# Optimization experiments

Measured on AMD Instinct MI355X. Metric: run time of the kernel, lower is better.

The kernel has to match this reference:

```python
import jax, jax.numpy as jnp
import numpy as np
import math

N_HEADS = 8
D_EMBED = 512
D_CROSS = 768
FF_DIM = 2048
D_HEAD = D_EMBED // N_HEADS


def _gelu_tanh(x):
    # matches the module's hand-written tanh GELU
    return 0.5 * x * (1.0 + jnp.tanh(jnp.sqrt(2.0 / jnp.pi) * (x + 0.044715 * x ** 3)))


def _layer_norm(x, g, b, eps=1e-5):
    mu = jnp.mean(x, axis=-1, keepdims=True)
    var = jnp.var(x, axis=-1, keepdims=True)
    return (x - mu) * jax.lax.rsqrt(var + eps) * g + b


def setup_inputs() -> dict:
    key = jax.random.key(0)
    ks = jax.random.split(key, 20)
    s = 0.02
    inp = {
        "x": jax.random.normal(ks[0], (2, 4096, D_EMBED), jnp.float32),
        "y": jax.random.normal(ks[1], (2, 77, D_CROSS), jnp.float32),
        # self-attention: fused in_proj [D, 3D]
        "sa_in_w": jax.random.normal(ks[2], (D_EMBED, 3 * D_EMBED), jnp.float32) * s,
        "sa_in_b": jnp.zeros((3 * D_EMBED,), jnp.float32),
        "sa_out_w": jax.random.normal(ks[3], (D_EMBED, D_EMBED), jnp.float32) * s,
        "sa_out_b": jnp.zeros((D_EMBED,), jnp.float32),
        # cross-attention
        "ca_q_w": jax.random.normal(ks[4], (D_EMBED, D_EMBED), jnp.float32) * s,
        "ca_q_b": jnp.zeros((D_EMBED,), jnp.float32),
        "ca_k_w": jax.random.normal(ks[5], (D_CROSS, D_EMBED), jnp.float32) * s,
        "ca_k_b": jnp.zeros((D_EMBED,), jnp.float32),
        "ca_v_w": jax.random.normal(ks[6], (D_CROSS, D_EMBED), jnp.float32) * s,
        "ca_v_b": jnp.zeros((D_EMBED,), jnp.float32),
        "ca_out_w": jax.random.normal(ks[7], (D_EMBED, D_EMBED), jnp.float32) * s,
        "ca_out_b": jnp.zeros((D_EMBED,), jnp.float32),
        # feed-forward
        "ff_w1": jax.random.normal(ks[8], (D_EMBED, FF_DIM), jnp.float32) * s,
        "ff_b1": jnp.zeros((FF_DIM,), jnp.float32),
        "ff_w2": jax.random.normal(ks[9], (FF_DIM, D_EMBED), jnp.float32) * s,
        "ff_b2": jnp.zeros((D_EMBED,), jnp.float32),
        # layer norms
        "ln1_g": jnp.ones((D_EMBED,), jnp.float32),
        "ln1_b": jnp.zeros((D_EMBED,), jnp.float32),
        "ln2_g": jnp.ones((D_EMBED,), jnp.float32),
        "ln2_b": jnp.zeros((D_EMBED,), jnp.float32),
        "ln3_g": jnp.ones((D_EMBED,), jnp.float32),
        "ln3_b": jnp.zeros((D_EMBED,), jnp.float32),
    }
    return inp


def _mha(q, k, v):
    # q,k,v: [B, S, D] -> split heads -> attention -> merge
    B, Sq, D = q.shape
    Skv = k.shape[1]
    qh = q.reshape(B, Sq, N_HEADS, D_HEAD).transpose(0, 2, 1, 3)
    kh = k.reshape(B, Skv, N_HEADS, D_HEAD).transpose(0, 2, 1, 3)
    vh = v.reshape(B, Skv, N_HEADS, D_HEAD).transpose(0, 2, 1, 3)
    scores = jnp.einsum("bhqd,bhkd->bhqk", qh, kh) / math.sqrt(D_HEAD)
    w = jax.nn.softmax(scores, axis=-1)
    out = jnp.einsum("bhqk,bhkd->bhqd", w, vh)
    return out.transpose(0, 2, 1, 3).reshape(B, Sq, D)


def reference(x, y, sa_in_w, sa_in_b, sa_out_w, sa_out_b,
              ca_q_w, ca_q_b, ca_k_w, ca_k_b, ca_v_w, ca_v_b, ca_out_w, ca_out_b,
              ff_w1, ff_b1, ff_w2, ff_b2,
              ln1_g, ln1_b, ln2_g, ln2_b, ln3_g, ln3_b):
    # self-attention (no causal mask; default causal_mask=False)
    qkv = x @ sa_in_w + sa_in_b
    q, k, v = jnp.split(qkv, 3, axis=-1)
    sa = _mha(q, k, v) @ sa_out_w + sa_out_b
    x = _layer_norm(x + sa, ln1_g, ln1_b)

    # cross-attention to y
    qc = x @ ca_q_w + ca_q_b
    kc = y @ ca_k_w + ca_k_b
    vc = y @ ca_v_w + ca_v_b
    ca = _mha(qc, kc, vc) @ ca_out_w + ca_out_b
    x = _layer_norm(x + ca, ln2_g, ln2_b)

    # feed-forward with tanh GELU
    ff = _gelu_tanh(x @ ff_w1 + ff_b1) @ ff_w2 + ff_b2
    x = _layer_norm(x + ff, ln3_g, ln3_b)
    return x
```

## Files before the change

### kernel.cpp

```cpp
#include <hip/hip_runtime.h>
#include <stdint.h>

typedef float floatx4 __attribute__((ext_vector_type(4)));
typedef __bf16 bf16x8 __attribute__((ext_vector_type(8)));
typedef unsigned int uintx4 __attribute__((ext_vector_type(4)));
typedef unsigned short ushort_t;

__device__ __forceinline__ float b2f(ushort_t u) {
  union { unsigned int i; float f; } x; x.i = ((unsigned int)u) << 16; return x.f;
}
__device__ __forceinline__ ushort_t f2b(float f) {
  union { float f; unsigned int i; } x; x.f = f;
  unsigned int i = x.i;
  return (ushort_t)((i + 0x7FFFu + ((i >> 16) & 1u)) >> 16);
}
__device__ __forceinline__ unsigned fbits(float f) {
  union { float f; unsigned u; } x; x.f = f; return x.u;
}
__device__ __forceinline__ uintx4 ld16(const void* p) {
  uintx4 v; __builtin_memcpy(&v, p, 16); return v;
}
__device__ __forceinline__ void st16(void* p, uintx4 v) { __builtin_memcpy(p, &v, 16); }
__device__ __forceinline__ floatx4 f4splat(float x) { floatx4 v = {x, x, x, x}; return v; }
__device__ __forceinline__ void sched_fence() { asm volatile("" ::: "memory"); }

__device__ __forceinline__ floatx4 mfma16(uintx4 a, uintx4 b, floatx4 c) {
  return __builtin_amdgcn_mfma_f32_16x16x32_bf16(
      __builtin_bit_cast(bf16x8, a), __builtin_bit_cast(bf16x8, b), c, 0, 0, 0);
}

__device__ __forceinline__ void gll16(const ushort_t* g, ushort_t* l) {
  __builtin_amdgcn_global_load_lds(
      (__attribute__((address_space(1))) void*)(g),
      (__attribute__((address_space(3))) void*)(l), 16, 0, 0);
}

template <int EPI>
__global__ __launch_bounds__(256, 2) void gemm_bt(
    const ushort_t* __restrict__ A, const ushort_t* __restrict__ Bt,
    const float* __restrict__ bias, void* __restrict__ Cout,
    int N, int K) {
  __shared__ alignas(16) ushort_t lA[128 * 32];
  __shared__ alignas(16) ushort_t lB[128 * 32];
  const int tid = threadIdx.x;
  const int wave = tid >> 6, lane = tid & 63;
  const int quad = lane >> 4, l16 = lane & 15;
  const int bm = blockIdx.y * 128, bn = blockIdx.x * 128;
  const int wm = (wave >> 1) * 64, wn = (wave & 1) * 64;

  const ushort_t* ag0 = A + (size_t)(bm + wave * 32 + (lane >> 2)) * K + (lane & 3) * 8;
  const ushort_t* ag1 = ag0 + (size_t)16 * K;
  const ushort_t* bg0 = Bt + (size_t)(bn + wave * 32 + (lane >> 2)) * K + (lane & 3) * 8;
  const ushort_t* bg1 = bg0 + (size_t)16 * K;
  ushort_t* la = lA + wave * 1024;
  ushort_t* lb = lB + wave * 1024;

  floatx4 acc[4][4];
#pragma unroll
  for (int i = 0; i < 4; i++)
#pragma unroll
    for (int j = 0; j < 4; j++) acc[i][j] = f4splat(0.f);

  for (int k0 = 0; k0 < K; k0 += 32) {
    __syncthreads();
    gll16(ag0 + k0, la);
    gll16(ag1 + k0, la + 512);
    gll16(bg0 + k0, lb);
    gll16(bg1 + k0, lb + 512);
    __syncthreads();
    uintx4 af[4], bf[4];
#pragma unroll
    for (int i = 0; i < 4; i++) af[i] = ld16(&lA[(wm + i * 16 + l16) * 32 + quad * 8]);
#pragma unroll
    for (int i = 0; i < 4; i++) bf[i] = ld16(&lB[(wn + i * 16 + l16) * 32 + quad * 8]);
#pragma unroll
    for (int mi = 0; mi < 4; mi++)
#pragma unroll
      for (int ni = 0; ni < 4; ni++) acc[mi][ni] = mfma16(af[mi], bf[ni], acc[mi][ni]);
  }

  float bv[4];
#pragma unroll
  for (int ni = 0; ni < 4; ni++) bv[ni] = bias[bn + wn + ni * 16 + l16];

#pragma unroll
  for (int mi = 0; mi < 4; mi++)
#pragma unroll
    for (int ni = 0; ni < 4; ni++)
#pragma unroll
      for (int r = 0; r < 4; r++) {
        int row = bm + wm + mi * 16 + quad * 4 + r;
        int col = bn + wn + ni * 16 + l16;
        float v = acc[mi][ni][r] + bv[ni];
        if (EPI == 2) {
          float w = v + 0.044715f * v * v * v;
          float e = __builtin_amdgcn_exp2f(-2.3022084f * w);
          v = v * __builtin_amdgcn_rcpf(1.f + e);
        }
        if (EPI == 1)
          ((float*)Cout)[(size_t)row * N + col] = v;
        else
          ((ushort_t*)Cout)[(size_t)row * N + col] = f2b(v);
      }
}

__global__ __launch_bounds__(256, 2) void flash_self(
    const ushort_t* __restrict__ qkv, const ushort_t* __restrict__ vt,
    ushort_t* __restrict__ outp) {
  __shared__ alignas(16) ushort_t lK[64 * 72];
  __shared__ alignas(16) ushort_t lV[64 * 72];
  __shared__ alignas(16) ushort_t lPT[4 * 32 * 72];
  const int tid = threadIdx.x, wave = tid >> 6, lane = tid & 63;
  const int quad = lane >> 4, l16 = lane & 15;
  const int bh = blockIdx.x, b = bh >> 3, h = bh & 7;
  const int qt = blockIdx.y;

  const ushort_t* Qb = qkv + (size_t)b * 4096 * 1536 + h * 64;
  const ushort_t* Kb = Qb + 512;
  const ushort_t* Vtb = vt + (size_t)bh * 64 * 4096;

  uintx4 qf[2][2];
#pragma unroll
  for (int mi = 0; mi < 2; mi++)
#pragma unroll
    for (int kf = 0; kf < 2; kf++)
      qf[mi][kf] = ld16(Qb + (size_t)(qt * 128 + wave * 32 + mi * 16 + l16) * 1536 +
                        kf * 32 + quad * 8);

  floatx4 O[2][4];
#pragma unroll
  for (int mi = 0; mi < 2; mi++)
#pragma unroll
    for (int dn = 0; dn < 4; dn++) O[mi][dn] = f4splat(0.f);
  float lsum[2] = {0.f, 0.f};
  const float c = 0.18033688f;

  const int sr0 = tid >> 3, sr1 = 32 + (tid >> 3), sc0 = (tid & 7) * 8;
  uintx4 kr0 = ld16(Kb + (size_t)sr0 * 1536 + sc0);
  uintx4 kr1 = ld16(Kb + (size_t)sr1 * 1536 + sc0);
  uintx4 vr0 = ld16(Vtb + (size_t)sr0 * 4096 + sc0);
  uintx4 vr1 = ld16(Vtb + (size_t)sr1 * 4096 + sc0);

  ushort_t* PTw = lPT + wave * 32 * 72;

  for (int kt = 0; kt < 64; kt++) {
    __syncthreads();
    st16(&lK[sr0 * 72 + sc0], kr0);
    st16(&lK[sr1 * 72 + sc0], kr1);
    st16(&lV[sr0 * 72 + sc0], vr0);
    st16(&lV[sr1 * 72 + sc0], vr1);
    __syncthreads();

    int ktn = (kt + 1) & 63;
    kr0 = ld16(Kb + (size_t)(ktn * 64 + sr0) * 1536 + sc0);
    kr1 = ld16(Kb + (size_t)(ktn * 64 + sr1) * 1536 + sc0);
    vr0 = ld16(Vtb + (size_t)sr0 * 4096 + ktn * 64 + sc0);
    vr1 = ld16(Vtb + (size_t)sr1 * 4096 + ktn * 64 + sc0);

    floatx4 S[2][4];
#pragma unroll
    for (int ni = 0; ni < 4; ni++) {
      uintx4 k0 = ld16(&lK[(ni * 16 + l16) * 72 + quad * 8]);
      uintx4 k1 = ld16(&lK[(ni * 16 + l16) * 72 + 32 + quad * 8]);
#pragma unroll
      for (int mi = 0; mi < 2; mi++) {
        floatx4 z = f4splat(0.f);
        z = mfma16(k0, qf[mi][0], z);
        z = mfma16(k1, qf[mi][1], z);
        S[mi][ni] = z;
      }
    }

#pragma unroll
    for (int mi = 0; mi < 2; mi++) {
      float rs = 0.f;
#pragma unroll
      for (int ni = 0; ni < 4; ni++) {
        float p0 = __builtin_amdgcn_exp2f(S[mi][ni][0] * c);
        float p1 = __builtin_amdgcn_exp2f(S[mi][ni][1] * c);
        float p2 = __builtin_amdgcn_exp2f(S[mi][ni][2] * c);
        float p3 = __builtin_amdgcn_exp2f(S[mi][ni][3] * c);
        rs += (p0 + p1) + (p2 + p3);
        unsigned dd[2];
        dd[0] = (fbits(p1) & 0xFFFF0000u) | (fbits(p0) >> 16);
        dd[1] = (fbits(p3) & 0xFFFF0000u) | (fbits(p2) >> 16);
        __builtin_memcpy(&PTw[(mi * 16 + l16) * 72 + ni * 16 + quad * 4], dd, 8);
      }
      lsum[mi] += rs;
    }
    sched_fence();

#pragma unroll
    for (int f = 0; f < 2; f++) {
      uintx4 pf0 = ld16(&PTw[(0 + l16) * 72 + f * 32 + quad * 8]);
      uintx4 pf1 = ld16(&PTw[(16 + l16) * 72 + f * 32 + quad * 8]);
#pragma unroll
      for (int dn = 0; dn < 4; dn++) {
        uintx4 vb = ld16(&lV[(dn * 16 + l16) * 72 + f * 32 + quad * 8]);
        O[0][dn] = mfma16(vb, pf0, O[0][dn]);
        O[1][dn] = mfma16(vb, pf1, O[1][dn]);
      }
    }
  }

#pragma unroll
  for (int mi = 0; mi < 2; mi++) {
    lsum[mi] += __shfl_xor(lsum[mi], 16);
    lsum[mi] += __shfl_xor(lsum[mi], 32);
  }

#pragma unroll
  for (int mi = 0; mi < 2; mi++) {
    float inv = 1.0f / lsum[mi];
    const size_t rowg = (size_t)b * 4096 + qt * 128 + wave * 32 + mi * 16 + l16;
#pragma unroll
    for (int dn = 0; dn < 4; dn++) {
      unsigned u0 = (unsigned)f2b(O[mi][dn][0] * inv) | ((unsigned)f2b(O[mi][dn][1] * inv) << 16);
      unsigned u1 = (unsigned)f2b(O[mi][dn][2] * inv) | ((unsigned)f2b(O[mi][dn][3] * inv) << 16);
      unsigned uu[2] = {u0, u1};
      __builtin_memcpy(outp + rowg * 512 + h * 64 + dn * 16 + quad * 4, uu, 8);
    }
  }
}

__global__ __launch_bounds__(256, 2) void cross_attn(
    const ushort_t* __restrict__ qc, const ushort_t* __restrict__ kc,
    const ushort_t* __restrict__ vc, ushort_t* __restrict__ outp) {
  __shared__ alignas(16) ushort_t lK[96 * 72];
  __shared__ alignas(16) ushort_t lV[64 * 104];
  __shared__ alignas(16) ushort_t lP[128 * 104];
  const int tid = threadIdx.x, wave = tid >> 6, lane = tid & 63;
  const int quad = lane >> 4, l16 = lane & 15;
  const int bh = blockIdx.y, b = bh >> 3, h = bh & 7;
  const int qt = blockIdx.x;

#pragma unroll
  for (int i = 0; i < 3; i++) {
    int ch = i * 256 + tid;
    int r = ch >> 3, c8 = ch & 7;
    uintx4 d = {0u, 0u, 0u, 0u};
    if (r < 77) d = ld16(kc + (size_t)(b * 77 + r) * 512 + h * 64 + c8 * 8);
    st16(&lK[r * 72 + c8 * 8], d);
  }
  for (int i = 0; i < 24; i++) {
    int e = i * 256 + tid;
    int dd = e / 96, s = e - dd * 96;
    ushort_t v = 0;
    if (s < 77) v = vc[(size_t)(b * 77 + s) * 512 + h * 64 + dd];
    lV[dd * 104 + s] = v;
  }
  __syncthreads();

  const int qr0 = qt * 128 + wave * 32;
  uintx4 qf[2][2];
#pragma unroll
  for (int mi = 0; mi < 2; mi++)
#pragma unroll
    for (int kf = 0; kf < 2; kf++)
      qf[mi][kf] =
          ld16(qc + (size_t)(b * 4096 + qr0 + mi * 16 + l16) * 512 + h * 64 + kf * 32 + quad * 8);

  floatx4 S[2][6];
#pragma unroll
  for (int ni = 0; ni < 6; ni++) {
    uintx4 k0 = ld16(&lK[(ni * 16 + l16) * 72 + quad * 8]);
    uintx4 k1 = ld16(&lK[(ni * 16 + l16) * 72 + 32 + quad * 8]);
#pragma unroll
    for (int mi = 0; mi < 2; mi++) {
      floatx4 z = f4splat(0.f);
      z = mfma16(qf[mi][0], k0, z);
      z = mfma16(qf[mi][1], k1, z);
      S[mi][ni] = z;
    }
  }
  const float c = 0.18033688f;
#pragma unroll
  for (int ni = 4; ni < 6; ni++)
    if (ni * 16 + l16 >= 77) {
      S[0][ni] = f4splat(-1e30f);
      S[1][ni] = f4splat(-1e30f);
    }

  floatx4 linv[2];
#pragma unroll
  for (int mi = 0; mi < 2; mi++) {
    floatx4 cm = S[mi][0];
#pragma unroll
    for (int ni = 1; ni < 6; ni++)
#pragma unroll
      for (int r = 0; r < 4; r++) cm[r] = fmaxf(cm[r], S[mi][ni][r]);
#pragma unroll
    for (int off = 1; off < 16; off <<= 1)
#pragma unroll
      for (int r = 0; r < 4; r++) cm[r] = fmaxf(cm[r], __shfl_xor(cm[r], off));
    floatx4 rs = f4splat(0.f);
#pragma unroll
    for (int ni = 0; ni < 6; ni++)
#pragma unroll
      for (int r = 0; r < 4; r++) {
        float p = __builtin_amdgcn_exp2f(S[mi][ni][r] * c - cm[r] * c);
        S[mi][ni][r] = p;
        rs[r] += p;
      }
#pragma unroll
    for (int off = 1; off < 16; off <<= 1)
#pragma unroll
      for (int r = 0; r < 4; r++) rs[r] += __shfl_xor(rs[r], off);
#pragma unroll
    for (int r = 0; r < 4; r++) linv[mi][r] = 1.0f / rs[r];
#pragma unroll
    for (int ni = 0; ni < 6; ni++)
#pragma unroll
      for (int r = 0; r < 4; r++)
        lP[(wave * 32 + mi * 16 + quad * 4 + r) * 104 + ni * 16 + l16] = f2b(S[mi][ni][r]);
  }
  sched_fence();

  floatx4 O[2][4];
#pragma unroll
  for (int mi = 0; mi < 2; mi++)
#pragma unroll
    for (int dn = 0; dn < 4; dn++) O[mi][dn] = f4splat(0.f);
#pragma unroll
  for (int kf = 0; kf < 3; kf++) {
    uintx4 pa0 = ld16(&lP[(wave * 32 + 0 + l16) * 104 + kf * 32 + quad * 8]);
    uintx4 pa1 = ld16(&lP[(wave * 32 + 16 + l16) * 104 + kf * 32 + quad * 8]);
#pragma unroll
    for (int dn = 0; dn < 4; dn++) {
      uintx4 vb = ld16(&lV[(dn * 16 + l16) * 104 + kf * 32 + quad * 8]);
      O[0][dn] = mfma16(pa0, vb, O[0][dn]);
      O[1][dn] = mfma16(pa1, vb, O[1][dn]);
    }
  }
#pragma unroll
  for (int mi = 0; mi < 2; mi++)
#pragma unroll
    for (int dn = 0; dn < 4; dn++)
#pragma unroll
      for (int r = 0; r < 4; r++) {
        int row = b * 4096 + qt * 128 + wave * 32 + mi * 16 + quad * 4 + r;
        int col = h * 64 + dn * 16 + l16;
        outp[(size_t)row * 512 + col] = f2b(O[mi][dn][r] * linv[mi][r]);
      }
}

template <int RESF>
__global__ __launch_bounds__(256) void ln_kernel(
    const float* __restrict__ p, const void* __restrict__ resv,
    const float* __restrict__ g, const float* __restrict__ bb,
    float* __restrict__ out32, ushort_t* __restrict__ outbf) {
  const int row = blockIdx.x * 4 + (threadIdx.x >> 6);
  const int lane = threadIdx.x & 63;
  const size_t base = (size_t)row * 512;
  float v[8];
  float s = 0.f, ss = 0.f;
#pragma unroll
  for (int i = 0; i < 4; i++) {
    int cidx = i * 128 + lane * 2;
    float2 pv; __builtin_memcpy(&pv, p + base + cidx, 8);
    float rx, ry;
    if (RESF) {
      float2 rv; __builtin_memcpy(&rv, (const float*)resv + base + cidx, 8);
      rx = rv.x; ry = rv.y;
    } else {
      unsigned int rr; __builtin_memcpy(&rr, (const ushort_t*)resv + base + cidx, 4);
      rx = b2f((ushort_t)(rr & 0xFFFFu));
      ry = b2f((ushort_t)(rr >> 16));
    }
    float a = pv.x + rx, b2 = pv.y + ry;
    v[2 * i] = a; v[2 * i + 1] = b2;
    s += a + b2;
    ss += a * a + b2 * b2;
  }
#pragma unroll
  for (int off = 1; off < 64; off <<= 1) {
    s += __shfl_xor(s, off);
    ss += __shfl_xor(ss, off);
  }
  float mean = s * (1.f / 512.f);
  float var = ss * (1.f / 512.f) - mean * mean;
  float rstd = rsqrtf(var + 1e-5f);
#pragma unroll
  for (int i = 0; i < 4; i++) {
    int cidx = i * 128 + lane * 2;
    float2 gv; __builtin_memcpy(&gv, g + cidx, 8);
    float2 bv; __builtin_memcpy(&bv, bb + cidx, 8);
    float y0 = (v[2 * i] - mean) * rstd * gv.x + bv.x;
    float y1 = (v[2 * i + 1] - mean) * rstd * gv.y + bv.y;
    if (out32) {
      float2 o; o.x = y0; o.y = y1;
      __builtin_memcpy(out32 + base + cidx, &o, 8);
    }
    if (outbf) {
      unsigned int o16 = (unsigned int)f2b(y0) | ((unsigned int)f2b(y1) << 16);
      __builtin_memcpy(outbf + base + cidx, &o16, 4);
    }
  }
}

__global__ __launch_bounds__(256) void small_gemm2(
    const float* __restrict__ y, const float* __restrict__ wk,
    const float* __restrict__ bk, const float* __restrict__ wv,
    const float* __restrict__ bv, ushort_t* __restrict__ kout,
    ushort_t* __restrict__ vout) {
  int bid = blockIdx.x;
  const float* W; const float* B; ushort_t* O;
  if (bid >= 308) { W = wv; B = bv; O = vout; bid -= 308; }
  else            { W = wk; B = bk; O = kout; }
  int idx = bid * 256 + threadIdx.x;
  if (idx >= 154 * 512) return;
  int r = idx >> 9, col = idx & 511;
  const float* ya = y + (size_t)r * 768;
  float acc = B[col];
#pragma unroll 4
  for (int k = 0; k < 768; k++) acc += ya[k] * W[(size_t)k * 512 + col];
  O[idx] = f2b(acc);
}

struct TransJob { const float* in; ushort_t* out; int ldi, ldo, nbx, start; };
struct TransJobs6 { TransJob j[6]; };

__global__ __launch_bounds__(256) void transpose6(TransJobs6 jobs) {
  __shared__ float t[32][33];
  int bid = blockIdx.x;
  int ji = 0;
#pragma unroll
  for (int i = 1; i < 6; i++)
    if (bid >= jobs.j[i].start) ji = i;
  TransJob J = jobs.j[ji];
  int local = bid - J.start;
  int by = local / J.nbx, bx = local - by * J.nbx;
  int r0 = by * 32, c0 = bx * 32;
  int tx = threadIdx.x & 31, ty = threadIdx.x >> 5;
#pragma unroll
  for (int i = 0; i < 4; i++)
    t[ty + 8 * i][tx] = J.in[(size_t)(r0 + ty + 8 * i) * J.ldi + c0 + tx];
  __syncthreads();
#pragma unroll
  for (int i = 0; i < 4; i++)
    J.out[(size_t)(c0 + ty + 8 * i) * J.ldo + r0 + tx] = f2b(t[tx][ty + 8 * i]);
}

__global__ __launch_bounds__(256) void xcvt(const float* __restrict__ in,
                                            ushort_t* __restrict__ out) {
  int i = (blockIdx.x * 256 + threadIdx.x) * 4;
  float4 v; __builtin_memcpy(&v, in + i, 16);
  ushort_t o[4] = {f2b(v.x), f2b(v.y), f2b(v.z), f2b(v.w)};
  __builtin_memcpy(out + i, o, 8);
}

__global__ __launch_bounds__(256) void transpose_v(const ushort_t* __restrict__ qkv,
                                                   ushort_t* __restrict__ vt) {
  __shared__ ushort_t t[32][33];
  int b = blockIdx.z;
  const ushort_t* in = qkv + (size_t)b * 4096 * 1536 + 1024;
  ushort_t* out = vt + (size_t)b * 512 * 4096;
  int r0 = blockIdx.y * 32, c0 = blockIdx.x * 32;
  int tx = threadIdx.x & 31, ty = threadIdx.x >> 5;
#pragma unroll
  for (int i = 0; i < 4; i++)
    t[ty + 8 * i][tx] = in[(size_t)(r0 + ty + 8 * i) * 1536 + c0 + tx];
  __syncthreads();
#pragma unroll
  for (int i = 0; i < 4; i++)
    out[(size_t)(c0 + ty + 8 * i) * 4096 + r0 + tx] = t[tx][ty + 8 * i];
}

extern "C" void kernel_launch(void* const* d_in, const int* in_sizes, int n_in,
                              void* d_out, int out_size, void* d_ws, size_t ws_size,
                              hipStream_t stream) {
  const size_t MiB = 1048576;
  if (ws_size < 64 * MiB) return;

  const float* x        = (const float*)d_in[0];
  const float* y        = (const float*)d_in[1];
  const float* sa_in_w  = (const float*)d_in[2];
  const float* sa_in_b  = (const float*)d_in[3];
  const float* sa_out_w = (const float*)d_in[4];
  const float* sa_out_b = (const float*)d_in[5];
  const float* ca_q_w   = (const float*)d_in[6];
  const float* ca_q_b   = (const float*)d_in[7];
  const float* ca_k_w   = (const float*)d_in[8];
  const float* ca_k_b   = (const float*)d_in[9];
  const float* ca_v_w   = (const float*)d_in[10];
  const float* ca_v_b   = (const float*)d_in[11];
  const float* ca_out_w = (const float*)d_in[12];
  const float* ca_out_b = (const float*)d_in[13];
  const float* ff_w1    = (const float*)d_in[14];
  const float* ff_b1    = (const float*)d_in[15];
  const float* ff_w2    = (const float*)d_in[16];
  const float* ff_b2    = (const float*)d_in[17];
  const float* ln1_g    = (const float*)d_in[18];
  const float* ln1_b    = (const float*)d_in[19];
  const float* ln2_g    = (const float*)d_in[20];
  const float* ln2_b    = (const float*)d_in[21];
  const float* ln3_g    = (const float*)d_in[22];
  const float* ln3_b    = (const float*)d_in[23];

  char* w = (char*)d_ws;
  ushort_t* QKV  = (ushort_t*)(w + 0);
  float*    P    = (float*)(w + 0);
  ushort_t* QC   = (ushort_t*)(w + 0);
  float*    P2   = (float*)(w + 0);
  ushort_t* FF   = (ushort_t*)(w + 0);
  ushort_t* ATT  = (ushort_t*)(w + 24 * MiB);
  ushort_t* VT   = (ushort_t*)(w + 32 * MiB);
  float*    XB0  = (float*)(w + 32 * MiB);
  float*    P3   = (float*)(w + 32 * MiB);
  ushort_t* XBF  = (ushort_t*)(w + 48 * MiB);
  ushort_t* XB0b = (ushort_t*)(w + 48 * MiB);
  ushort_t* XB1b = (ushort_t*)(w + 48 * MiB);
  ushort_t* WT   = (ushort_t*)(w + 56 * MiB);
  ushort_t* KC   = (ushort_t*)(w + 63 * MiB);
  ushort_t* VC   = KC + 154 * 512;

  ushort_t* WT_sain  = WT;
  ushort_t* WT_saout = WT_sain + 786432;
  ushort_t* WT_caq   = WT_saout + 262144;
  ushort_t* WT_caout = WT_caq + 262144;
  ushort_t* WT_ff1   = WT_caout + 262144;
  ushort_t* WT_ff2   = WT_ff1 + 1048576;

  TransJobs6 tj;
  tj.j[0] = TransJob{sa_in_w,  WT_sain,  1536, 512, 48, 0};
  tj.j[1] = TransJob{sa_out_w, WT_saout, 512,  512, 16, 768};
  tj.j[2] = TransJob{ca_q_w,   WT_caq,   512,  512, 16, 1024};
  tj.j[3] = TransJob{ca_out_w, WT_caout, 512,  512, 16, 1280};
  tj.j[4] = TransJob{ff_w1,    WT_ff1,   2048, 512, 64, 1536};
  tj.j[5] = TransJob{ff_w2,    WT_ff2,   512, 2048, 16, 2560};
  transpose6<<<3584, 256, 0, stream>>>(tj);
  xcvt<<<4096, 256, 0, stream>>>(x, XBF);

  gemm_bt<0><<<dim3(12, 64), 256, 0, stream>>>(XBF, WT_sain, sa_in_b, QKV, 1536, 512);
  transpose_v<<<dim3(16, 128, 2), 256, 0, stream>>>(QKV, VT);
  flash_self<<<dim3(16, 32), 256, 0, stream>>>(QKV, VT, ATT);
  gemm_bt<1><<<dim3(4, 64), 256, 0, stream>>>(ATT, WT_saout, sa_out_b, P, 512, 512);
  ln_kernel<1><<<2048, 256, 0, stream>>>(P, x, ln1_g, ln1_b, XB0, XB0b);

  gemm_bt<0><<<dim3(4, 64), 256, 0, stream>>>(XB0b, WT_caq, ca_q_b, QC, 512, 512);
  small_gemm2<<<616, 256, 0, stream>>>(y, ca_k_w, ca_k_b, ca_v_w, ca_v_b, KC, VC);
  cross_attn<<<dim3(32, 16), 256, 0, stream>>>(QC, KC, VC, ATT);
  gemm_bt<1><<<dim3(4, 64), 256, 0, stream>>>(ATT, WT_caout, ca_out_b, P2, 512, 512);
  ln_kernel<1><<<2048, 256, 0, stream>>>(P2, XB0, ln2_g, ln2_b, nullptr, XB1b);

  gemm_bt<2><<<dim3(16, 64), 256, 0, stream>>>(XB1b, WT_ff1, ff_b1, FF, 2048, 512);
  gemm_bt<1><<<dim3(4, 64), 256, 0, stream>>>(FF, WT_ff2, ff_b2, P3, 512, 2048);
  ln_kernel<0><<<2048, 256, 0, stream>>>(P3, XB1b, ln3_g, ln3_b, (float*)d_out, nullptr);
}
```

Baseline: 466.8 us.

## Pre-pack K/V into MFMA fragment layout, narrow GEMM tiles, vectorize layernorm

Self-attention K and V are repacked by two new kernels into per-lane MFMA fragment order, so flash_self loads fragments straight from global memory and drops its LDS staging and both per-tile barriers. The N=512 GEMMs switch to a 64-wide N tile, which doubles the grid to 512 blocks and fills the GPU better. Layernorm now uses 16-byte loads and stores. In exchange there are two extra packing launches and more global traffic in the attention inner loop, now served through cache instead of LDS.

```diff
diff --git a/kernel.cpp b/kernel.cpp
--- a/kernel.cpp
+++ b/kernel.cpp
@@ -35,58 +35,67 @@
       (__attribute__((address_space(3))) void*)(l), 16, 0, 0);
 }
 
-template <int EPI>
+template <int EPI, int NT>
 __global__ __launch_bounds__(256, 2) void gemm_bt(
     const ushort_t* __restrict__ A, const ushort_t* __restrict__ Bt,
     const float* __restrict__ bias, void* __restrict__ Cout,
     int N, int K) {
+  constexpr int NI = NT / 32;
   __shared__ alignas(16) ushort_t lA[128 * 32];
-  __shared__ alignas(16) ushort_t lB[128 * 32];
+  __shared__ alignas(16) ushort_t lB[NT * 32];
   const int tid = threadIdx.x;
   const int wave = tid >> 6, lane = tid & 63;
   const int quad = lane >> 4, l16 = lane & 15;
-  const int bm = blockIdx.y * 128, bn = blockIdx.x * 128;
-  const int wm = (wave >> 1) * 64, wn = (wave & 1) * 64;
+  const int bm = blockIdx.y * 128, bn = blockIdx.x * NT;
+  const int wm = (wave >> 1) * 64, wn = (wave & 1) * (NT / 2);
 
   const ushort_t* ag0 = A + (size_t)(bm + wave * 32 + (lane >> 2)) * K + (lane & 3) * 8;
   const ushort_t* ag1 = ag0 + (size_t)16 * K;
-  const ushort_t* bg0 = Bt + (size_t)(bn + wave * 32 + (lane >> 2)) * K + (lane & 3) * 8;
-  const ushort_t* bg1 = bg0 + (size_t)16 * K;
   ushort_t* la = lA + wave * 1024;
-  ushort_t* lb = lB + wave * 1024;
-
-  floatx4 acc[4][4];
+  const ushort_t* bg0;
+  const ushort_t* bg1 = nullptr;
+  ushort_t* lb;
+  if (NT == 128) {
+    bg0 = Bt + (size_t)(bn + wave * 32 + (lane >> 2)) * K + (lane & 3) * 8;
+    bg1 = bg0 + (size_t)16 * K;
+    lb = lB + wave * 1024;
+  } else {
+    bg0 = Bt + (size_t)(bn + wave * 16 + (lane >> 2)) * K + (lane & 3) * 8;
+    lb = lB + wave * 512;
+  }
+
+  floatx4 acc[4][NI];
 #pragma unroll
   for (int i = 0; i < 4; i++)
 #pragma unroll
-    for (int j = 0; j < 4; j++) acc[i][j] = f4splat(0.f);
+    for (int j = 0; j < NI; j++) acc[i][j] = f4splat(0.f);
 
   for (int k0 = 0; k0 < K; k0 += 32) {
     __syncthreads();
     gll16(ag0 + k0, la);
     gll16(ag1 + k0, la + 512);
     gll16(bg0 + k0, lb);
-    gll16(bg1 + k0, lb + 512);
+    if (NT == 128) gll16(bg1 + k0, lb + 512);
     __syncthreads();
-    uintx4 af[4], bf[4];
+    uintx4 af[4], bf[NI];
 #pragma unroll
     for (int i = 0; i < 4; i++) af[i] = ld16(&lA[(wm + i * 16 + l16) * 32 + quad * 8]);
 #pragma unroll
-    for (int i = 0; i < 4; i++) bf[i] = ld16(&lB[(wn + i * 16 + l16) * 32 + quad * 8]);
+    for (int i = 0; i < NI; i++) bf[i] = ld16(&lB[(wn + i * 16 + l16) * 32 + quad * 8]);
 #pragma unroll
     for (int mi = 0; mi < 4; mi++)
 #pragma unroll
-      for (int ni = 0; ni < 4; ni++) acc[mi][ni] = mfma16(af[mi], bf[ni], acc[mi][ni]);
-  }
-
-  float bv[4];
-#pragma unroll
-  for (int ni = 0; ni < 4; ni++) bv[ni] = bias[bn + wn + ni * 16 + l16];
+      for (int ni = 0; ni < NI; ni++) acc[mi][ni] = mfma16(af[mi], bf[ni], acc[mi][ni]);
+  }
+
+  float bv[NI];
+#pragma unroll
+  for (int ni = 0; ni < NI; ni++) bv[ni] = bias[bn + wn + ni * 16 + l16];
 
 #pragma unroll
   for (int mi = 0; mi < 4; mi++)
 #pragma unroll
-    for (int ni = 0; ni < 4; ni++)
+    for (int ni = 0; ni < NI; ni++)
 #pragma unroll
       for (int r = 0; r < 4; r++) {
         int row = bm + wm + mi * 16 + quad * 4 + r;
@@ -104,11 +113,52 @@
       }
 }
 
+__global__ __launch_bounds__(256) void pack_k(const ushort_t* __restrict__ qkv,
+                                              ushort_t* __restrict__ KP) {
+  int g = blockIdx.x * 256 + threadIdx.x;
+  int lane = g & 63;
+  int frag = (g >> 6) & 7;
+  int kt = (g >> 9) & 63;
+  int bh = g >> 15;
+  int b = bh >> 3, h = bh & 7;
+  int ni = frag >> 1, kf = frag & 1;
+  int l16 = lane & 15, quad = lane >> 4;
+  const ushort_t* src = qkv + (size_t)(b * 4096 + kt * 64 + ni * 16 + l16) * 1536 +
+                        512 + h * 64 + kf * 32 + quad * 8;
+  st16(KP + (size_t)g * 8, ld16(src));
+}
+
+__global__ __launch_bounds__(256) void pack_v(const ushort_t* __restrict__ qkv,
+                                              ushort_t* __restrict__ VP) {
+  __shared__ ushort_t t[64 * 72];
+  int bh = blockIdx.x, kt = blockIdx.y;
+  int b = bh >> 3, h = bh & 7;
+  int tid = threadIdx.x;
+#pragma unroll
+  for (int i = 0; i < 2; i++) {
+    int c = i * 256 + tid;
+    int row = c >> 3, c8 = (c & 7) * 8;
+    uintx4 d4 = ld16(qkv + (size_t)(b * 4096 + kt * 64 + row) * 1536 + 1024 + h * 64 + c8);
+    ushort_t tmp[8];
+    __builtin_memcpy(tmp, &d4, 16);
+#pragma unroll
+    for (int j = 0; j < 8; j++) t[(c8 + j) * 72 + row] = tmp[j];
+  }
+  __syncthreads();
+#pragma unroll
+  for (int i = 0; i < 2; i++) {
+    int c = i * 256 + tid;
+    int frag = c >> 6, lane = c & 63;
+    int f = frag >> 2, dn = frag & 3;
+    int l16 = lane & 15, quad = lane >> 4;
+    uintx4 d4 = ld16(&t[(dn * 16 + l16) * 72 + f * 32 + quad * 8]);
+    st16(VP + ((size_t)(bh * 64 + kt) * 8 + frag) * 512 + (size_t)lane * 8, d4);
+  }
+}
+
 __global__ __launch_bounds__(256, 2) void flash_self(
-    const ushort_t* __restrict__ qkv, const ushort_t* __restrict__ vt,
-    ushort_t* __restrict__ outp) {
-  __shared__ alignas(16) ushort_t lK[64 * 72];
-  __shared__ alignas(16) ushort_t lV[64 * 72];
+    const ushort_t* __restrict__ qkv, const ushort_t* __restrict__ KP,
+    const ushort_t* __restrict__ VP, ushort_t* __restrict__ outp) {
   __shared__ alignas(16) ushort_t lPT[4 * 32 * 72];
   const int tid = threadIdx.x, wave = tid >> 6, lane = tid & 63;
   const int quad = lane >> 4, l16 = lane & 15;
@@ -116,8 +166,8 @@
   const int qt = blockIdx.y;
 
   const ushort_t* Qb = qkv + (size_t)b * 4096 * 1536 + h * 64;
-  const ushort_t* Kb = Qb + 512;
-  const ushort_t* Vtb = vt + (size_t)bh * 64 * 4096;
+  const ushort_t* KPb = KP + (size_t)bh * 64 * 4096;
+  const ushort_t* VPb = VP + (size_t)bh * 64 * 4096;
 
   uintx4 qf[2][2];
 #pragma unroll
@@ -134,42 +184,36 @@
     for (int dn = 0; dn < 4; dn++) O[mi][dn] = f4splat(0.f);
   float lsum[2] = {0.f, 0.f};
   const float c = 0.18033688f;
-
-  const int sr0 = tid >> 3, sr1 = 32 + (tid >> 3), sc0 = (tid & 7) * 8;
-  uintx4 kr0 = ld16(Kb + (size_t)sr0 * 1536 + sc0);
-  uintx4 kr1 = ld16(Kb + (size_t)sr1 * 1536 + sc0);
-  uintx4 vr0 = ld16(Vtb + (size_t)sr0 * 4096 + sc0);
-  uintx4 vr1 = ld16(Vtb + (size_t)sr1 * 4096 + sc0);
-
   ushort_t* PTw = lPT + wave * 32 * 72;
 
+#pragma unroll 2
   for (int kt = 0; kt < 64; kt++) {
-    __syncthreads();
-    st16(&lK[sr0 * 72 + sc0], kr0);
-    st16(&lK[sr1 * 72 + sc0], kr1);
-    st16(&lV[sr0 * 72 + sc0], vr0);
-    st16(&lV[sr1 * 72 + sc0], vr1);
-    __syncthreads();
-
-    int ktn = (kt + 1) & 63;
-    kr0 = ld16(Kb + (size_t)(ktn * 64 + sr0) * 1536 + sc0);
-    kr1 = ld16(Kb + (size_t)(ktn * 64 + sr1) * 1536 + sc0);
-    vr0 = ld16(Vtb + (size_t)sr0 * 4096 + ktn * 64 + sc0);
-    vr1 = ld16(Vtb + (size_t)sr1 * 4096 + ktn * 64 + sc0);
+    const ushort_t* kb = KPb + kt * 4096;
+    uintx4 kfr[4][2];
+#pragma unroll
+    for (int ni = 0; ni < 4; ni++)
+#pragma unroll
+      for (int kf = 0; kf < 2; kf++)
+        kfr[ni][kf] = ld16(kb + ((ni * 2 + kf) * 64 + lane) * 8);
 
     floatx4 S[2][4];
 #pragma unroll
-    for (int ni = 0; ni < 4; ni++) {
-      uintx4 k0 = ld16(&lK[(ni * 16 + l16) * 72 + quad * 8]);
-      uintx4 k1 = ld16(&lK[(ni * 16 + l16) * 72 + 32 + quad * 8]);
+    for (int ni = 0; ni < 4; ni++)
 #pragma unroll
       for (int mi = 0; mi < 2; mi++) {
         floatx4 z = f4splat(0.f);
-        z = mfma16(k0, qf[mi][0], z);
-        z = mfma16(k1, qf[mi][1], z);
+        z = mfma16(kfr[ni][0], qf[mi][0], z);
+        z = mfma16(kfr[ni][1], qf[mi][1], z);
         S[mi][ni] = z;
       }
-    }
+
+    const ushort_t* vbp = VPb + kt * 4096;
+    uintx4 vf[2][4];
+#pragma unroll
+    for (int f = 0; f < 2; f++)
+#pragma unroll
+      for (int dn = 0; dn < 4; dn++)
+        vf[f][dn] = ld16(vbp + ((f * 4 + dn) * 64 + lane) * 8);
 
 #pragma unroll
     for (int mi = 0; mi < 2; mi++) {
@@ -196,9 +240,8 @@
       uintx4 pf1 = ld16(&PTw[(16 + l16) * 72 + f * 32 + quad * 8]);
 #pragma unroll
       for (int dn = 0; dn < 4; dn++) {
-        uintx4 vb = ld16(&lV[(dn * 16 + l16) * 72 + f * 32 + quad * 8]);
-        O[0][dn] = mfma16(vb, pf0, O[0][dn]);
-        O[1][dn] = mfma16(vb, pf1, O[1][dn]);
+        O[0][dn] = mfma16(vf[f][dn], pf0, O[0][dn]);
+        O[1][dn] = mfma16(vf[f][dn], pf1, O[1][dn]);
       }
     }
   }
@@ -355,22 +398,26 @@
   float v[8];
   float s = 0.f, ss = 0.f;
 #pragma unroll
-  for (int i = 0; i < 4; i++) {
-    int cidx = i * 128 + lane * 2;
-    float2 pv; __builtin_memcpy(&pv, p + base + cidx, 8);
-    float rx, ry;
+  for (int i = 0; i < 2; i++) {
+    int cidx = i * 256 + lane * 4;
+    float4 pv; __builtin_memcpy(&pv, p + base + cidx, 16);
+    float rv[4];
     if (RESF) {
-      float2 rv; __builtin_memcpy(&rv, (const float*)resv + base + cidx, 8);
-      rx = rv.x; ry = rv.y;
+      __builtin_memcpy(rv, (const float*)resv + base + cidx, 16);
     } else {
-      unsigned int rr; __builtin_memcpy(&rr, (const ushort_t*)resv + base + cidx, 4);
-      rx = b2f((ushort_t)(rr & 0xFFFFu));
-      ry = b2f((ushort_t)(rr >> 16));
-    }
-    float a = pv.x + rx, b2 = pv.y + ry;
-    v[2 * i] = a; v[2 * i + 1] = b2;
-    s += a + b2;
-    ss += a * a + b2 * b2;
+      ushort_t rr[4];
+      __builtin_memcpy(rr, (const ushort_t*)resv + base + cidx, 8);
+#pragma unroll
+      for (int j = 0; j < 4; j++) rv[j] = b2f(rr[j]);
+    }
+    float pvv[4] = {pv.x, pv.y, pv.z, pv.w};
+#pragma unroll
+    for (int j = 0; j < 4; j++) {
+      float a = pvv[j] + rv[j];
+      v[i * 4 + j] = a;
+      s += a;
+      ss += a * a;
+    }
   }
 #pragma unroll
   for (int off = 1; off < 64; off <<= 1) {
@@ -381,19 +428,18 @@
   float var = ss * (1.f / 512.f) - mean * mean;
   float rstd = rsqrtf(var + 1e-5f);
 #pragma unroll
-  for (int i = 0; i < 4; i++) {
-    int cidx = i * 128 + lane * 2;
-    float2 gv; __builtin_memcpy(&gv, g + cidx, 8);
-    float2 bv; __builtin_memcpy(&bv, bb + cidx, 8);
-    float y0 = (v[2 * i] - mean) * rstd * gv.x + bv.x;
-    float y1 = (v[2 * i + 1] - mean) * rstd * gv.y + bv.y;
-    if (out32) {
-      float2 o; o.x = y0; o.y = y1;
-      __builtin_memcpy(out32 + base + cidx, &o, 8);
-    }
+  for (int i = 0; i < 2; i++) {
+    int cidx = i * 256 + lane * 4;
+    float gv[4], bv2[4];
+    __builtin_memcpy(gv, g + cidx, 16);
+    __builtin_memcpy(bv2, bb + cidx, 16);
+    float y[4];
+#pragma unroll
+    for (int j = 0; j < 4; j++) y[j] = (v[i * 4 + j] - mean) * rstd * gv[j] + bv2[j];
+    if (out32) __builtin_memcpy(out32 + base + cidx, y, 16);
     if (outbf) {
-      unsigned int o16 = (unsigned int)f2b(y0) | ((unsigned int)f2b(y1) << 16);
-      __builtin_memcpy(outbf + base + cidx, &o16, 4);
+      ushort_t o[4] = {f2b(y[0]), f2b(y[1]), f2b(y[2]), f2b(y[3])};
+      __builtin_memcpy(outbf + base + cidx, o, 8);
     }
   }
 }
@@ -447,23 +493,6 @@
   float4 v; __builtin_memcpy(&v, in + i, 16);
   ushort_t o[4] = {f2b(v.x), f2b(v.y), f2b(v.z), f2b(v.w)};
   __builtin_memcpy(out + i, o, 8);
-}
-
-__global__ __launch_bounds__(256) void transpose_v(const ushort_t* __restrict__ qkv,
-                                                   ushort_t* __restrict__ vt) {
-  __shared__ ushort_t t[32][33];
-  int b = blockIdx.z;
-  const ushort_t* in = qkv + (size_t)b * 4096 * 1536 + 1024;
-  ushort_t* out = vt + (size_t)b * 512 * 4096;
-  int r0 = blockIdx.y * 32, c0 = blockIdx.x * 32;
-  int tx = threadIdx.x & 31, ty = threadIdx.x >> 5;
-#pragma unroll
-  for (int i = 0; i < 4; i++)
-    t[ty + 8 * i][tx] = in[(size_t)(r0 + ty + 8 * i) * 1536 + c0 + tx];
-  __syncthreads();
-#pragma unroll
-  for (int i = 0; i < 4; i++)
-    out[(size_t)(c0 + ty + 8 * i) * 4096 + r0 + tx] = t[tx][ty + 8 * i];
 }
 
 extern "C" void kernel_launch(void* const* d_in, const int* in_sizes, int n_in,
@@ -504,7 +533,8 @@
   float*    P2   = (float*)(w + 0);
   ushort_t* FF   = (ushort_t*)(w + 0);
   ushort_t* ATT  = (ushort_t*)(w + 24 * MiB);
-  ushort_t* VT   = (ushort_t*)(w + 32 * MiB);
+  ushort_t* KP   = (ushort_t*)(w + 32 * MiB);
+  ushort_t* VP   = (ushort_t*)(w + 40 * MiB);
   float*    XB0  = (float*)(w + 32 * MiB);
   float*    P3   = (float*)(w + 32 * MiB);
   ushort_t* XBF  = (ushort_t*)(w + 48 * MiB);
@@ -531,19 +561,20 @@
   transpose6<<<3584, 256, 0, stream>>>(tj);
   xcvt<<<4096, 256, 0, stream>>>(x, XBF);
 
-  gemm_bt<0><<<dim3(12, 64), 256, 0, stream>>>(XBF, WT_sain, sa_in_b, QKV, 1536, 512);
-  transpose_v<<<dim3(16, 128, 2), 256, 0, stream>>>(QKV, VT);
-  flash_self<<<dim3(16, 32), 256, 0, stream>>>(QKV, VT, ATT);
-  gemm_bt<1><<<dim3(4, 64), 256, 0, stream>>>(ATT, WT_saout, sa_out_b, P, 512, 512);
+  gemm_bt<0, 128><<<dim3(12, 64), 256, 0, stream>>>(XBF, WT_sain, sa_in_b, QKV, 1536, 512);
+  pack_k<<<2048, 256, 0, stream>>>(QKV, KP);
+  pack_v<<<dim3(16, 64), 256, 0, stream>>>(QKV, VP);
+  flash_self<<<dim3(16, 32), 256, 0, stream>>>(QKV, KP, VP, ATT);
+  gemm_bt<1, 64><<<dim3(8, 64), 256, 0, stream>>>(ATT, WT_saout, sa_out_b, P, 512, 512);
   ln_kernel<1><<<2048, 256, 0, stream>>>(P, x, ln1_g, ln1_b, XB0, XB0b);
 
-  gemm_bt<0><<<dim3(4, 64), 256, 0, stream>>>(XB0b, WT_caq, ca_q_b, QC, 512, 512);
+  gemm_bt<0, 64><<<dim3(8, 64), 256, 0, stream>>>(XB0b, WT_caq, ca_q_b, QC, 512, 512);
   small_gemm2<<<616, 256, 0, stream>>>(y, ca_k_w, ca_k_b, ca_v_w, ca_v_b, KC, VC);
   cross_attn<<<dim3(32, 16), 256, 0, stream>>>(QC, KC, VC, ATT);
-  gemm_bt<1><<<dim3(4, 64), 256, 0, stream>>>(ATT, WT_caout, ca_out_b, P2, 512, 512);
+  gemm_bt<1, 64><<<dim3(8, 64), 256, 0, stream>>>(ATT, WT_caout, ca_out_b, P2, 512, 512);
   ln_kernel<1><<<2048, 256, 0, stream>>>(P2, XB0, ln2_g, ln2_b, nullptr, XB1b);
 
-  gemm_bt<2><<<dim3(16, 64), 256, 0, stream>>>(XB1b, WT_ff1, ff_b1, FF, 2048, 512);
-  gemm_bt<1><<<dim3(4, 64), 256, 0, stream>>>(FF, WT_ff2, ff_b2, P3, 512, 2048);
+  gemm_bt<2, 128><<<dim3(16, 64), 256, 0, stream>>>(XB1b, WT_ff1, ff_b1, FF, 2048, 512);
+  gemm_bt<1, 64><<<dim3(8, 64), 256, 0, stream>>>(FF, WT_ff2, ff_b2, P3, 512, 2048);
   ln_kernel<0><<<2048, 256, 0, stream>>>(P3, XB1b, ln3_g, ln3_b, (float*)d_out, nullptr);
 }
```

After: 441.3 us. 1.06x faster.
